# Performance work log

Measured on AMD Instinct MI355X. Metric: run time of the kernel, lower is better.

## Reference

```python
import jax, jax.numpy as jnp
import numpy as np

B, N, D, K = 8, 2048, 3, 16
CIN, CD, COUT = 64, 16, 128
C = CIN + CD            # 80, channels after concat
DM = 2                  # depth_multiplier = ceil(128/80)
EPS = 1e-5


def _bn(x, g, b):
    # BatchNorm1d in training mode: biased batch stats over axis 0
    m = x.mean(0)
    v = x.var(0)
    return (x - m) * jax.lax.rsqrt(v + EPS) * g + b


def setup_inputs() -> dict:
    key = jax.random.key(0)
    ks = jax.random.split(key, 12)
    f = lambda k, shp: (jax.random.normal(k, shp, jnp.float32) * 0.05)
    return dict(
        x=jax.random.normal(ks[0], (B, N, CIN), jnp.float32),
        pos=jax.random.normal(ks[1], (B, N, D), jnp.float32),
        # mlp1: Linear(D,CD) ELU BN, Linear(CD,CD) ELU BN
        W1=f(ks[2], (D, CD)), b1=jnp.zeros((CD,)), g1=jnp.ones((CD,)), be1=jnp.zeros((CD,)),
        W2=f(ks[3], (CD, CD)), b2=jnp.zeros((CD,)), g2=jnp.ones((CD,)), be2=jnp.zeros((CD,)),
        # mlp2: Linear(D*K,K^2) ELU BN, grouped Conv1d(K,K^2,K) ELU BN, grouped Conv1d BN
        Wl=f(ks[4], (D * K, K * K)), bl=jnp.zeros((K * K,)), gl=jnp.ones((K * K,)), bel=jnp.zeros((K * K,)),
        WcA=f(ks[5], (K, K, K)), bcA=jnp.zeros((K, K)), gA=jnp.ones((K * K,)), beA=jnp.zeros((K * K,)),
        WcB=f(ks[6], (K, K, K)), bcB=jnp.zeros((K, K)), gB=jnp.ones((K * K,)), beB=jnp.zeros((K * K,)),
        # final depthwise Conv1d(C, C*DM, K, groups=C) + Linear(C*DM, COUT)
        Wd=f(ks[7], (C, DM, K)), bd=jnp.zeros((C, DM)),
        Wo=f(ks[8], (C * DM, COUT)), bo=jnp.zeros((COUT,)),
    )


def reference(x, pos, W1, b1, g1, be1, W2, b2, g2, be2,
              Wl, bl, gl, bel, WcA, bcA, gA, beA, WcB, bcB, gB, beB,
              Wd, bd, Wo, bo):
    # --- KNN via squared pairwise distances (same ordering as torch.cdist) ---
    sq = jnp.sum(pos * pos, -1)                                     # (B,N)
    d2 = sq[:, :, None] + sq[:, None, :] - 2.0 * jnp.einsum('bnd,bmd->bnm', pos, pos)
    _, idx = jax.lax.top_k(-d2, K)                                  # (B,N,K) nearest (incl. self)
    gather = jax.vmap(lambda a, i: a[i])                            # batched fancy-gather
    pos_j = gather(pos, idx)                                        # (B,N,K,D)
    d = pos[:, :, None, :] - pos_j                                  # relative coords (B,N,K,D)

    # --- mlp1 over B*N*K points -> lifted features x_star ---
    h = d.reshape(-1, D)                                            # (BNK,D)
    h = _bn(jax.nn.elu(h @ W1 + b1), g1, be1)
    h = _bn(jax.nn.elu(h @ W2 + b2), g2, be2)                       # (BNK,CD)

    xj = gather(x, idx)                                             # (B,N,K,CIN)
    xs = jnp.concatenate([h.reshape(B, N, K, CD), xj], -1)          # (B,N,K,C)
    xs = xs.reshape(B * N, K, C).transpose(0, 2, 1)                 # (BN,C,K)

    # --- mlp2: learned KxK transform from relative coords ---
    t = d.reshape(B * N, K * D)
    t = _bn(jax.nn.elu(t @ Wl + bl), gl, bel).reshape(-1, K, K)
    # grouped Conv1d(K, K^2, K, groups=K): out[b,g,o] = sum_k t[b,g,k]*W[g,o,k] + bias[g,o]
    t = jax.nn.elu(jnp.einsum('bgk,gok->bgo', t, WcA) + bcA)
    t = _bn(t.reshape(-1, K * K), gA, beA).reshape(-1, K, K)
    t = jnp.einsum('bgk,gok->bgo', t, WcB) + bcB
    t = _bn(t.reshape(-1, K * K), gB, beB).reshape(-1, K, K)        # (BN,K,K)

    # --- apply transform, depthwise conv, final linear ---
    xt = jnp.einsum('bck,bko->bco', xs, t)                          # (BN,C,K)
    o = jnp.einsum('bck,cmk->bcm', xt, Wd) + bd                     # (BN,C,DM)
    o = o.reshape(B * N, C * DM) @ Wo + bo                          # (BN,COUT)
    return o.reshape(B, N, COUT)
```

## Files before the change

### kernel.cpp

```cpp
#include <hip/hip_runtime.h>
#include <math.h>

#define NN 2048
#define KNbr 16
#define BNpts 16384
#define BNKr  262144

__device__ __forceinline__ float eluf(float v) { return v > 0.f ? v : expm1f(v); }

__global__ __launch_bounds__(256) void knn_kernel(const float* __restrict__ pos,
                                                  int* __restrict__ idxout,
                                                  float* __restrict__ drel) {
  int wav = threadIdx.x >> 6, lane = threadIdx.x & 63;
  int bn = blockIdx.x*4 + wav;
  int b = bn >> 11, n = bn & (NN - 1);
  const float* pb = pos + (size_t)b * NN * 3;
  float qx = pb[n*3], qy = pb[n*3+1], qz = pb[n*3+2];
  float sqn = __fadd_rn(__fadd_rn(__fmul_rn(qx,qx), __fmul_rn(qy,qy)), __fmul_rn(qz,qz));
  double kreg[32];
#pragma unroll
  for (int s = 0; s < 32; ++s) {
    int m = s*64 + lane;
    float px = pb[m*3], py = pb[m*3+1], pz = pb[m*3+2];
    float sqm = __fadd_rn(__fadd_rn(__fmul_rn(px,px), __fmul_rn(py,py)), __fmul_rn(pz,pz));
    float dot = __fmaf_rn(qz, pz, __fmaf_rn(qy, py, __fmul_rn(qx, px)));
    float d2  = __fsub_rn(__fadd_rn(sqn, sqm), __fmul_rn(2.0f, dot));
    unsigned int bits = __float_as_uint(d2);
    unsigned int uf = bits ^ (((unsigned int)((int)bits >> 31)) >> 1);
    kreg[s] = __hiloint2double((int)uf, m);
  }
  const double KINF = __hiloint2double(0x7FF00000, 0);
  for (int k = 0; k < KNbr; ++k) {
    double g0 = fmin(fmin(kreg[0],  kreg[1]),  fmin(kreg[2],  kreg[3]));
    double g1 = fmin(fmin(kreg[4],  kreg[5]),  fmin(kreg[6],  kreg[7]));
    double g2 = fmin(fmin(kreg[8],  kreg[9]),  fmin(kreg[10], kreg[11]));
    double g3 = fmin(fmin(kreg[12], kreg[13]), fmin(kreg[14], kreg[15]));
    double g4 = fmin(fmin(kreg[16], kreg[17]), fmin(kreg[18], kreg[19]));
    double g5 = fmin(fmin(kreg[20], kreg[21]), fmin(kreg[22], kreg[23]));
    double g6 = fmin(fmin(kreg[24], kreg[25]), fmin(kreg[26], kreg[27]));
    double g7 = fmin(fmin(kreg[28], kreg[29]), fmin(kreg[30], kreg[31]));
    double bk = fmin(fmin(fmin(g0, g1), fmin(g2, g3)),
                     fmin(fmin(g4, g5), fmin(g6, g7)));
#pragma unroll
    for (int off = 32; off > 0; off >>= 1) {
      double ok = __shfl_xor(bk, off);
      bk = fmin(bk, ok);
    }
    int fi = __builtin_amdgcn_readfirstlane(__double2loint(bk));
    if (lane == 0) {
      idxout[bn*KNbr + k] = fi;
      drel[(size_t)(bn*KNbr + k)*3 + 0] = __fsub_rn(qx, pb[fi*3+0]);
      drel[(size_t)(bn*KNbr + k)*3 + 1] = __fsub_rn(qy, pb[fi*3+1]);
      drel[(size_t)(bn*KNbr + k)*3 + 2] = __fsub_rn(qz, pb[fi*3+2]);
    }
    bool owner = (lane == (fi & 63));
#define CLR(i) case i: if (owner) kreg[i] = KINF; break;
    switch (fi >> 6) {
      CLR(0)  CLR(1)  CLR(2)  CLR(3)  CLR(4)  CLR(5)  CLR(6)  CLR(7)
      CLR(8)  CLR(9)  CLR(10) CLR(11) CLR(12) CLR(13) CLR(14) CLR(15)
      CLR(16) CLR(17) CLR(18) CLR(19) CLR(20) CLR(21) CLR(22) CLR(23)
      CLR(24) CLR(25) CLR(26) CLR(27) CLR(28) CLR(29) CLR(30) CLR(31)
    }
#undef CLR
  }
}

__global__ __launch_bounds__(256) void s1a_kernel(const float* __restrict__ drel,
                                                  const float* __restrict__ W1,
                                                  const float* __restrict__ b1,
                                                  double* __restrict__ part1) {
  __shared__ float sW[64];
  int tid = threadIdx.x;
  if (tid < 48) sW[tid] = W1[tid];
  if (tid < 16) sW[48+tid] = b1[tid];
  __syncthreads();
  const float* src = drel + (size_t)(blockIdx.x*256 + tid)*3;
  float a0 = src[0], a1 = src[1], a2 = src[2];
  float s[16], s2[16];
#pragma unroll
  for (int c = 0; c < 16; ++c) {
    float v = a0*sW[c] + a1*sW[16+c] + a2*sW[32+c] + sW[48+c];
    float e = eluf(v);
    s[c] = e; s2[c] = e*e;
  }
  __shared__ float wred[4][32];
  int lane = tid & 63, wav = tid >> 6;
#pragma unroll
  for (int j = 0; j < 32; ++j) {
    float v = (j < 16) ? s[j] : s2[j-16];
    for (int sh = 32; sh > 0; sh >>= 1) v += __shfl_down(v, sh);
    if (lane == 0) wred[wav][j] = v;
  }
  __syncthreads();
  if (tid < 32)
    part1[(size_t)blockIdx.x*32 + tid] =
      (double)wred[0][tid] + (double)wred[1][tid] + (double)wred[2][tid] + (double)wred[3][tid];
}

__global__ __launch_bounds__(256) void bn16_kernel(const double* __restrict__ part,
                                                   const float* __restrict__ g,
                                                   const float* __restrict__ be,
                                                   float* __restrict__ outp) {
  __shared__ double red[8][32];
  int t = threadIdx.x;
  int j = t & 31, grp = t >> 5;
  double v = 0.0;
#pragma unroll 4
  for (int bk = grp; bk < 1024; bk += 8) v += part[(size_t)bk*32 + j];
  red[grp][j] = v;
  __syncthreads();
  if (t < 32) {
    double s = 0.0;
    for (int gq = 0; gq < 8; ++gq) s += red[gq][t];
    red[0][t] = s;
  }
  __syncthreads();
  if (t < 16) {
    double S = red[0][t], S2 = red[0][16 + t];
    double m = S/262144.0, var = S2/262144.0 - m*m;
    double sc = (double)g[t]/sqrt(var + 1e-5);
    outp[t]      = (float)sc;
    outp[16 + t] = (float)((double)be[t] - m*sc);
  }
}

__global__ __launch_bounds__(256) void s1b_kernel(const float* __restrict__ drel,
                                                  const float* __restrict__ W1,
                                                  const float* __restrict__ b1,
                                                  const float* __restrict__ W2,
                                                  const float* __restrict__ b2,
                                                  const float* __restrict__ bn1p,
                                                  double* __restrict__ part2) {
  int tid = threadIdx.x;
  __shared__ float fsc1[16], fsh1[16];
  __shared__ float sW[64];
  __shared__ float sW2t[256];
  if (tid < 16) { fsc1[tid] = bn1p[tid]; fsh1[tid] = bn1p[16 + tid]; }
  if (tid < 48) sW[tid] = W1[tid];
  if (tid < 16) sW[48+tid] = b1[tid];
  sW2t[tid] = W2[(tid & 15)*16 + (tid >> 4)];
  __syncthreads();
  const float* src = drel + (size_t)(blockIdx.x*256 + tid)*3;
  float a0 = src[0], a1 = src[1], a2 = src[2];
  float s[16], s2[16];
  float y[16];
#pragma unroll
  for (int c = 0; c < 16; ++c) {
    float v = a0*sW[c] + a1*sW[16+c] + a2*sW[32+c] + sW[48+c];
    y[c] = eluf(v)*fsc1[c] + fsh1[c];
  }
#pragma unroll
  for (int c2 = 0; c2 < 16; ++c2) {
    float v = b2[c2];
    const float4* w4 = (const float4*)&sW2t[c2*16];
#pragma unroll
    for (int j4 = 0; j4 < 4; ++j4) {
      float4 ww = w4[j4];
      v += y[j4*4]*ww.x + y[j4*4+1]*ww.y + y[j4*4+2]*ww.z + y[j4*4+3]*ww.w;
    }
    float e = eluf(v);
    s[c2] = e; s2[c2] = e*e;
  }
  __shared__ float wred[4][32];
  int lane = tid & 63, wav = tid >> 6;
#pragma unroll
  for (int j = 0; j < 32; ++j) {
    float v = (j < 16) ? s[j] : s2[j-16];
    for (int sh = 32; sh > 0; sh >>= 1) v += __shfl_down(v, sh);
    if (lane == 0) wred[wav][j] = v;
  }
  __syncthreads();
  if (tid < 32)
    part2[(size_t)blockIdx.x*32 + tid] =
      (double)wred[0][tid] + (double)wred[1][tid] + (double)wred[2][tid] + (double)wred[3][tid];
}

__global__ __launch_bounds__(256) void s2l_kernel(const float* __restrict__ drel,
                                                  const float* __restrict__ Wl,
                                                  const float* __restrict__ bl,
                                                  float* __restrict__ tL,
                                                  double* __restrict__ partL) {
  __shared__ float srows[16*48];
  int tid = threadIdx.x;
  const float* src = drel + (size_t)blockIdx.x * 768;
  for (int i = tid; i < 768; i += 256) srows[i] = src[i];
  float w[48];
#pragma unroll
  for (int j = 0; j < 48; ++j) w[j] = Wl[j*256 + tid];
  float bias = bl[tid];
  __syncthreads();
  double s = 0.0, s2 = 0.0;
  for (int r = 0; r < 16; ++r) {
    float v = bias;
    const float4* sr = (const float4*)&srows[r*48];
#pragma unroll
    for (int j4 = 0; j4 < 12; ++j4) {
      float4 a4 = sr[j4];
      v += a4.x*w[j4*4] + a4.y*w[j4*4+1] + a4.z*w[j4*4+2] + a4.w*w[j4*4+3];
    }
    float e = eluf(v);
    tL[(size_t)(blockIdx.x*16 + r)*256 + tid] = e;
    double ed = (double)e;
    s += ed; s2 += ed*ed;
  }
  partL[(size_t)blockIdx.x*512 + tid]       = s;
  partL[(size_t)blockIdx.x*512 + 256 + tid] = s2;
}

__global__ __launch_bounds__(256) void pre512_kernel(const double* __restrict__ part,
                                                     double* __restrict__ partS) {
  int t = threadIdx.x;
  const double* p = part + (size_t)blockIdx.x*4*512;
  double a0 = 0.0, a1 = 0.0;
#pragma unroll
  for (int r = 0; r < 4; ++r) {
    a0 += p[r*512 + t];
    a1 += p[r*512 + 256 + t];
  }
  partS[(size_t)blockIdx.x*512 + t]       = a0;
  partS[(size_t)blockIdx.x*512 + 256 + t] = a1;
}

__global__ __launch_bounds__(1024) void bnred_kernel(const double* __restrict__ part,
                                                     const float* __restrict__ g,
                                                     const float* __restrict__ be,
                                                     float* __restrict__ bnp) {
  __shared__ double red[1024];
  int t = threadIdx.x;
  int c = t & 255, half = (t >> 8) & 1, q = t >> 9;
  const double* p = part + (size_t)(q*128)*512 + half*256 + c;
  double v = 0.0;
#pragma unroll 4
  for (int bk = 0; bk < 128; ++bk) v += p[(size_t)bk*512];
  red[t] = v;
  __syncthreads();
  if (t < 256) {
    double S  = red[t]       + red[512 + t];
    double S2 = red[256 + t] + red[768 + t];
    double m = S/16384.0, var = S2/16384.0 - m*m;
    double sc = (double)g[t]/sqrt(var + 1e-5);
    bnp[t]       = (float)sc;
    bnp[256 + t] = (float)((double)be[t] - m*sc);
  }
}

template<int DO_ELU>
__global__ __launch_bounds__(256) void s2conv_kernel(const float* __restrict__ bnIn,
                                                     const float* __restrict__ Wc,
                                                     const float* __restrict__ bc,
                                                     float* __restrict__ tBuf,
                                                     double* __restrict__ partOut) {
  int tid = threadIdx.x;
  float sc = bnIn[tid], sh = bnIn[256 + tid];
  int g = tid >> 4, o = tid & 15;
  float w[16];
#pragma unroll
  for (int k = 0; k < 16; ++k) w[k] = Wc[g*256 + o*16 + k];
  float bias = bc[tid];
  __shared__ float sin_[16*256];
  float* buf = tBuf + (size_t)blockIdx.x*16*256;
  for (int rr = 0; rr < 16; ++rr)
    sin_[rr*256 + tid] = buf[rr*256 + tid]*sc + sh;
  __syncthreads();
  double s = 0.0, s2 = 0.0;
  for (int rr = 0; rr < 16; ++rr) {
    float v = bias;
    const float4* row4 = (const float4*)&sin_[rr*256 + g*16];
#pragma unroll
    for (int k4 = 0; k4 < 4; ++k4) {
      float4 a4 = row4[k4];
      v += a4.x*w[k4*4] + a4.y*w[k4*4+1] + a4.z*w[k4*4+2] + a4.w*w[k4*4+3];
    }
    float e = DO_ELU ? eluf(v) : v;
    buf[rr*256 + tid] = e;
    double ed = (double)e;
    s += ed; s2 += ed*ed;
  }
  partOut[(size_t)blockIdx.x*512 + tid]       = s;
  partOut[(size_t)blockIdx.x*512 + 256 + tid] = s2;
}

__global__ __launch_bounds__(256) void final_kernel(const float* __restrict__ x,
                                                    const int* __restrict__ idxbuf,
                                                    const float* __restrict__ drel,
                                                    const float* __restrict__ tB,
                                                    const float* __restrict__ bnp,
                                                    const float* __restrict__ W1,
                                                    const float* __restrict__ b1,
                                                    const float* __restrict__ W2,
                                                    const float* __restrict__ b2,
                                                    const float* __restrict__ Wd,
                                                    const float* __restrict__ bd,
                                                    const float* __restrict__ Wo,
                                                    const float* __restrict__ bo,
                                                    float* __restrict__ out) {
  int tid = threadIdx.x;
  int bn0 = blockIdx.x*4;
  int b = bn0 >> 11;
  __shared__ float sbn1[32], sbn2[32];
  __shared__ float sBs[256], sBh[256];
  __shared__ int   sidx[64];
  __shared__ float sdrel[192];
  __shared__ float sW1[48], sb1[16], sb2[16];
  __shared__ float sW2t[256];
  __shared__ float tmat[1024];
  __shared__ float hs[4][16][17];
  __shared__ float xst[4][16][80];
  __shared__ float ovs[4][160];
  if (tid < 32) { sbn1[tid] = bnp[tid]; sbn2[tid] = bnp[32 + tid]; }
  sBs[tid] = bnp[64 + tid];
  sBh[tid] = bnp[320 + tid];
  if (tid < 64) sidx[tid] = idxbuf[bn0*16 + tid];
  if (tid < 192) sdrel[tid] = drel[(size_t)bn0*48 + tid];
  if (tid < 48) sW1[tid] = W1[tid];
  if (tid < 16) { sb1[tid] = b1[tid]; sb2[tid] = b2[tid]; }
  sW2t[tid] = W2[(tid & 15)*16 + (tid >> 4)];
  __syncthreads();
  for (int i = tid; i < 1024; i += 256) {
    int c = i & 255;
    tmat[i] = tB[(size_t)bn0*256 + i]*sBs[c] + sBh[c];
  }
  for (int i = tid; i < 1024; i += 256) {
    int pt = i >> 8, k = (i >> 4) & 15, c = i & 15;
    float a0 = sdrel[pt*48 + k*3], a1 = sdrel[pt*48 + k*3 + 1], a2 = sdrel[pt*48 + k*3 + 2];
    float v = a0*sW1[c] + a1*sW1[16+c] + a2*sW1[32+c] + sb1[c];
    hs[pt][k][c] = eluf(v)*sbn1[c] + sbn1[16+c];
  }
  __syncthreads();
  for (int i = tid; i < 1024; i += 256) {
    int pt = i >> 8, k = (i >> 4) & 15, c2 = i & 15;
    float v = sb2[c2];
    const float4* w4 = (const float4*)&sW2t[c2*16];
    float* hrow = &hs[pt][k][0];
#pragma unroll
    for (int j4 = 0; j4 < 4; ++j4) {
      float4 ww = w4[j4];
      v += hrow[j4*4]*ww.x + hrow[j4*4+1]*ww.y + hrow[j4*4+2]*ww.z + hrow[j4*4+3]*ww.w;
    }
    xst[pt][k][c2] = eluf(v)*sbn2[c2] + sbn2[16+c2];
  }
  for (int i = tid; i < 1024; i += 256) {
    int pt = i >> 8, k = (i >> 4) & 15, c4 = i & 15;
    float4 xv = *(const float4*)&x[((size_t)b*NN + sidx[pt*16 + k])*64 + c4*4];
    *(float4*)&xst[pt][k][16 + c4*4] = xv;
  }
  __syncthreads();
  if (tid < 160) {
    int pt = (tid >= 80) ? 1 : 0;
    int c = tid - pt*80;
    float xtr0[16], xtr1[16];
#pragma unroll
    for (int o = 0; o < 16; ++o) { xtr0[o] = 0.f; xtr1[o] = 0.f; }
#pragma unroll
    for (int k = 0; k < 16; ++k) {
      float xv0 = xst[pt][k][c];
      float xv1 = xst[pt + 2][k][c];
      const float* tm0 = &tmat[pt*256 + k*16];
      const float* tm1 = &tmat[(pt + 2)*256 + k*16];
#pragma unroll
      for (int o = 0; o < 16; ++o) {
        xtr0[o] += xv0*tm0[o];
        xtr1[o] += xv1*tm1[o];
      }
    }
    float b0 = bd[c*2], b1v = bd[c*2 + 1];
    float v00 = b0, v01 = b1v, v10 = b0, v11 = b1v;
#pragma unroll
    for (int k = 0; k < 16; ++k) {
      float w0 = Wd[c*32 + k], w1 = Wd[c*32 + 16 + k];
      v00 += xtr0[k]*w0; v01 += xtr0[k]*w1;
      v10 += xtr1[k]*w0; v11 += xtr1[k]*w1;
    }
    ovs[pt][c*2]       = v00;
    ovs[pt][c*2 + 1]   = v01;
    ovs[pt+2][c*2]     = v10;
    ovs[pt+2][c*2 + 1] = v11;
  }
  __syncthreads();
  {
    int pt0 = tid >> 7, co = tid & 127;
    float v0 = bo[co], v1 = v0;
#pragma unroll 8
    for (int i = 0; i < 160; ++i) {
      float wv = Wo[i*128 + co];
      v0 += ovs[pt0][i]*wv;
      v1 += ovs[pt0 + 2][i]*wv;
    }
    out[(size_t)(bn0 + pt0)*128 + co]     = v0;
    out[(size_t)(bn0 + pt0 + 2)*128 + co] = v1;
  }
}

extern "C" void kernel_launch(void* const* d_in, const int* in_sizes, int n_in,
                              void* d_out, int out_size, void* d_ws, size_t ws_size,
                              hipStream_t stream) {
  (void)in_sizes; (void)n_in; (void)out_size; (void)ws_size;
  const float* x   = (const float*)d_in[0];
  const float* pos = (const float*)d_in[1];
  const float* W1  = (const float*)d_in[2];
  const float* b1  = (const float*)d_in[3];
  const float* g1  = (const float*)d_in[4];
  const float* be1 = (const float*)d_in[5];
  const float* W2  = (const float*)d_in[6];
  const float* b2  = (const float*)d_in[7];
  const float* g2  = (const float*)d_in[8];
  const float* be2 = (const float*)d_in[9];
  const float* Wl  = (const float*)d_in[10];
  const float* bl  = (const float*)d_in[11];
  const float* gl  = (const float*)d_in[12];
  const float* bel = (const float*)d_in[13];
  const float* WcA = (const float*)d_in[14];
  const float* bcA = (const float*)d_in[15];
  const float* gA  = (const float*)d_in[16];
  const float* beA = (const float*)d_in[17];
  const float* WcB = (const float*)d_in[18];
  const float* bcB = (const float*)d_in[19];
  const float* gB  = (const float*)d_in[20];
  const float* beB = (const float*)d_in[21];
  const float* Wd  = (const float*)d_in[22];
  const float* bd  = (const float*)d_in[23];
  const float* Wo  = (const float*)d_in[24];
  const float* bo  = (const float*)d_in[25];
  float* out = (float*)d_out;

  char* ws = (char*)d_ws;
  int*    idxbuf = (int*)ws;
  float*  drel   = (float*)(ws + (1u<<20));
  float*  bufX   = (float*)(ws + (4u<<20));
  double* part1  = (double*)(ws + (20u<<20));
  double* part2  = (double*)(ws + (20u<<20) + (256u<<10));
  double* P      = (double*)(ws + (20u<<20) + (512u<<10));
  double* S      = (double*)(ws + (24u<<20) + (512u<<10));
  float*  bnp    = (float*)(ws + (25u<<20) + (512u<<10));
  float*  bnpL   = (float*)(ws + (25u<<20) + (512u<<10) + 4096);
  float*  bnpA   = (float*)(ws + (25u<<20) + (512u<<10) + 8192);

  knn_kernel<<<dim3(4096), dim3(256), 0, stream>>>(pos, idxbuf, drel);
  s1a_kernel<<<dim3(1024), dim3(256), 0, stream>>>(drel, W1, b1, part1);
  bn16_kernel<<<dim3(1), dim3(256), 0, stream>>>(part1, g1, be1, bnp + 0);
  s1b_kernel<<<dim3(1024), dim3(256), 0, stream>>>(drel, W1, b1, W2, b2, bnp + 0, part2);
  bn16_kernel<<<dim3(1), dim3(256), 0, stream>>>(part2, g2, be2, bnp + 32);
  s2l_kernel<<<dim3(1024), dim3(256), 0, stream>>>(drel, Wl, bl, bufX, P);
  pre512_kernel<<<dim3(256), dim3(256), 0, stream>>>(P, S);
  bnred_kernel<<<dim3(1), dim3(1024), 0, stream>>>(S, gl, bel, bnpL);
  s2conv_kernel<1><<<dim3(1024), dim3(256), 0, stream>>>(bnpL, WcA, bcA, bufX, P);
  pre512_kernel<<<dim3(256), dim3(256), 0, stream>>>(P, S);
  bnred_kernel<<<dim3(1), dim3(1024), 0, stream>>>(S, gA, beA, bnpA);
  s2conv_kernel<0><<<dim3(1024), dim3(256), 0, stream>>>(bnpA, WcB, bcB, bufX, P);
  pre512_kernel<<<dim3(256), dim3(256), 0, stream>>>(P, S);
  bnred_kernel<<<dim3(1), dim3(1024), 0, stream>>>(S, gB, beB, bnp + 64);
  final_kernel<<<dim3(4096), dim3(256), 0, stream>>>(x, idxbuf, drel, bufX, bnp,
                                                     W1, b1, W2, b2, Wd, bd, Wo, bo, out);
}
```

Baseline: 299.0 us.

## Split final kernel and batch the output linear over 32 points per block

The final kernel is split in two. The first part writes the per-point depthwise conv outputs (160 values per point) to a workspace buffer. A second kernel then computes the 160x128 output linear for 32 points per block, so each Wo load is reused across 16 points per thread instead of 2. This cuts global Wo traffic and increases arithmetic intensity, at the cost of an extra launch and a round trip of about 10 MB through memory.

```diff
diff --git a/kernel.cpp b/kernel.cpp
--- a/kernel.cpp
+++ b/kernel.cpp
@@ -280,20 +280,18 @@
   partOut[(size_t)blockIdx.x*512 + 256 + tid] = s2;
 }
 
-__global__ __launch_bounds__(256) void final_kernel(const float* __restrict__ x,
-                                                    const int* __restrict__ idxbuf,
-                                                    const float* __restrict__ drel,
-                                                    const float* __restrict__ tB,
-                                                    const float* __restrict__ bnp,
-                                                    const float* __restrict__ W1,
-                                                    const float* __restrict__ b1,
-                                                    const float* __restrict__ W2,
-                                                    const float* __restrict__ b2,
-                                                    const float* __restrict__ Wd,
-                                                    const float* __restrict__ bd,
-                                                    const float* __restrict__ Wo,
-                                                    const float* __restrict__ bo,
-                                                    float* __restrict__ out) {
+__global__ __launch_bounds__(256) void final1_kernel(const float* __restrict__ x,
+                                                     const int* __restrict__ idxbuf,
+                                                     const float* __restrict__ drel,
+                                                     const float* __restrict__ tB,
+                                                     const float* __restrict__ bnp,
+                                                     const float* __restrict__ W1,
+                                                     const float* __restrict__ b1,
+                                                     const float* __restrict__ W2,
+                                                     const float* __restrict__ b2,
+                                                     const float* __restrict__ Wd,
+                                                     const float* __restrict__ bd,
+                                                     float* __restrict__ ovbuf) {
   int tid = threadIdx.x;
   int bn0 = blockIdx.x*4;
   int b = bn0 >> 11;
@@ -306,7 +304,6 @@
   __shared__ float tmat[1024];
   __shared__ float hs[4][16][17];
   __shared__ float xst[4][16][80];
-  __shared__ float ovs[4][160];
   if (tid < 32) { sbn1[tid] = bnp[tid]; sbn2[tid] = bnp[32 + tid]; }
   sBs[tid] = bnp[64 + tid];
   sBh[tid] = bnp[320 + tid];
@@ -371,24 +368,49 @@
       v00 += xtr0[k]*w0; v01 += xtr0[k]*w1;
       v10 += xtr1[k]*w0; v11 += xtr1[k]*w1;
     }
-    ovs[pt][c*2]       = v00;
-    ovs[pt][c*2 + 1]   = v01;
-    ovs[pt+2][c*2]     = v10;
-    ovs[pt+2][c*2 + 1] = v11;
-  }
-  __syncthreads();
-  {
-    int pt0 = tid >> 7, co = tid & 127;
-    float v0 = bo[co], v1 = v0;
-#pragma unroll 8
-    for (int i = 0; i < 160; ++i) {
-      float wv = Wo[i*128 + co];
-      v0 += ovs[pt0][i]*wv;
-      v1 += ovs[pt0 + 2][i]*wv;
-    }
-    out[(size_t)(bn0 + pt0)*128 + co]     = v0;
-    out[(size_t)(bn0 + pt0 + 2)*128 + co] = v1;
-  }
+    ovbuf[(size_t)(bn0 + pt)*160 + c*2]       = v00;
+    ovbuf[(size_t)(bn0 + pt)*160 + c*2 + 1]   = v01;
+    ovbuf[(size_t)(bn0 + pt + 2)*160 + c*2]     = v10;
+    ovbuf[(size_t)(bn0 + pt + 2)*160 + c*2 + 1] = v11;
+  }
+}
+
+__global__ __launch_bounds__(256) void final2_kernel(const float* __restrict__ ovbuf,
+                                                     const float* __restrict__ Wo,
+                                                     const float* __restrict__ bo,
+                                                     float* __restrict__ out) {
+  __shared__ float ovt[32][164];
+  int tid = threadIdx.x;
+  int p0 = blockIdx.x*32;
+  const float* src = ovbuf + (size_t)p0*160;
+  for (int idx = tid; idx < 5120; idx += 256) {
+    int p = idx / 160;
+    int i = idx - p*160;
+    ovt[p][i] = src[idx];
+  }
+  __syncthreads();
+  int co = tid & 127, ph = tid >> 7;
+  float bv = bo[co];
+  float accs[16];
+#pragma unroll
+  for (int q = 0; q < 16; ++q) accs[q] = bv;
+  for (int i4 = 0; i4 < 40; ++i4) {
+    int i = i4*4;
+    float w0 = Wo[i*128 + co];
+    float w1 = Wo[(i+1)*128 + co];
+    float w2 = Wo[(i+2)*128 + co];
+    float w3 = Wo[(i+3)*128 + co];
+#pragma unroll
+    for (int q = 0; q < 16; ++q) {
+      const float4 a = *(const float4*)&ovt[ph*16 + q][i];
+      float acc = accs[q];
+      acc += a.x*w0; acc += a.y*w1; acc += a.z*w2; acc += a.w*w3;
+      accs[q] = acc;
+    }
+  }
+#pragma unroll
+  for (int q = 0; q < 16; ++q)
+    out[(size_t)(p0 + ph*16 + q)*128 + co] = accs[q];
 }
 
 extern "C" void kernel_launch(void* const* d_in, const int* in_sizes, int n_in,
@@ -434,6 +456,7 @@
   float*  bnp    = (float*)(ws + (25u<<20) + (512u<<10));
   float*  bnpL   = (float*)(ws + (25u<<20) + (512u<<10) + 4096);
   float*  bnpA   = (float*)(ws + (25u<<20) + (512u<<10) + 8192);
+  float*  ovbuf  = (float*)(ws + (26u<<20));
 
   knn_kernel<<<dim3(4096), dim3(256), 0, stream>>>(pos, idxbuf, drel);
   s1a_kernel<<<dim3(1024), dim3(256), 0, stream>>>(drel, W1, b1, part1);
@@ -449,6 +472,7 @@
   s2conv_kernel<0><<<dim3(1024), dim3(256), 0, stream>>>(bnpA, WcB, bcB, bufX, P);
   pre512_kernel<<<dim3(256), dim3(256), 0, stream>>>(P, S);
   bnred_kernel<<<dim3(1), dim3(1024), 0, stream>>>(S, gB, beB, bnp + 64);
-  final_kernel<<<dim3(4096), dim3(256), 0, stream>>>(x, idxbuf, drel, bufX, bnp,
-                                                     W1, b1, W2, b2, Wd, bd, Wo, bo, out);
-}
+  final1_kernel<<<dim3(4096), dim3(256), 0, stream>>>(x, idxbuf, drel, bufX, bnp,
+                                                      W1, b1, W2, b2, Wd, bd, ovbuf);
+  final2_kernel<<<dim3(512), dim3(256), 0, stream>>>(ovbuf, Wo, bo, out);
+}
```

After: 298.4 us (median of 2 runs). No clear change (-0.2%).
